# Kernel tuning notes

Hardware: AMD Instinct MI355X
Metric: run time of the kernel (lower is better)

The kernel has to match this reference:

```python
import jax, jax.numpy as jnp
import numpy as np

N = 50000   # number_of_nodes
E = 800000  # edges
K = 3       # Chebyshev order
C_IN = 64
C_OUT = 64


def _laplacian_weights(src, dst, w):
    # PyG ChebConv sym normalization with lambda_max=2: L_hat = -D^{-1/2} A D^{-1/2}
    deg = jax.ops.segment_sum(w, src, num_segments=N)
    dis = jnp.where(deg > 0, jax.lax.rsqrt(jnp.maximum(deg, 1e-12)), 0.0)
    return -dis[src] * w * dis[dst]


def _cheb(x, src, dst, lw, W, b):
    # x: [N, Cin], W: [K, Cin, Cout], b: [Cout]
    def prop(t):  # sparse L_hat @ t via gather + segment-sum scatter
        return jax.ops.segment_sum(lw[:, None] * t[src], dst, num_segments=N)
    Tx0 = x
    out = Tx0 @ W[0]
    Tx1 = prop(Tx0)
    out = out + Tx1 @ W[1]
    for k in range(2, W.shape[0]):  # Chebyshev recursion T_k = 2 L T_{k-1} - T_{k-2}
        Tx2 = 2.0 * prop(Tx1) - Tx0
        out = out + Tx2 @ W[k]
        Tx0, Tx1 = Tx1, Tx2
    return out + b


def setup_inputs() -> dict:
    key = jax.random.key(0)
    ks = jax.random.split(key, 20)
    inp = {
        "X": jax.random.normal(ks[0], (N, C_IN), jnp.float32),
        "edge_index": jax.random.randint(ks[1], (2, E), 0, N, jnp.int64),
        "edge_weight": jax.random.uniform(ks[2], (E,), jnp.float32),
        "H": jax.random.normal(ks[3], (N, C_OUT), jnp.float32),
    }
    names = ["xz", "hz", "xr", "hr", "xh", "hh"]
    for i, n in enumerate(names):
        cin = C_IN if n[0] == "x" else C_OUT
        inp[f"W_{n}"] = 0.1 * jax.random.normal(ks[4 + i], (K, cin, C_OUT), jnp.float32)
        inp[f"b_{n}"] = 0.1 * jax.random.normal(ks[10 + i], (C_OUT,), jnp.float32)
    return inp


def reference(X, edge_index, edge_weight, H,
              W_xz, W_hz, W_xr, W_hr, W_xh, W_hh,
              b_xz, b_hz, b_xr, b_hr, b_xh, b_hh):
    src, dst = edge_index[0], edge_index[1]
    lw = _laplacian_weights(src, dst, edge_weight)
    Z = jax.nn.sigmoid(_cheb(X, src, dst, lw, W_xz, b_xz) +
                       _cheb(H, src, dst, lw, W_hz, b_hz))
    R = jax.nn.sigmoid(_cheb(X, src, dst, lw, W_xr, b_xr) +
                       _cheb(H, src, dst, lw, W_hr, b_hr))
    H_tilde = jnp.tanh(_cheb(X, src, dst, lw, W_xh, b_xh) +
                       _cheb(H * R, src, dst, lw, W_hh, b_hh))
    H_new = Z * H + (1.0 - Z) * H_tilde
    return H_new
```

## Files before the change

kernel.cpp:

```cpp
#include <hip/hip_runtime.h>
#include <math.h>

#define CH 64

typedef __attribute__((ext_vector_type(8))) short bf16x8;
typedef __attribute__((ext_vector_type(4))) float f32x4;

static __device__ __forceinline__ float bf2f(ushort u) {
    union { unsigned int i; float f; } v; v.i = ((unsigned int)u) << 16; return v.f;
}
static __device__ __forceinline__ ushort f2bf(float f) {
    union { float f; unsigned int i; } v; v.f = f;
    unsigned int lsb = (v.i >> 16) & 1;
    v.i += 0x7fffu + lsb;
    return (ushort)(v.i >> 16);
}
static __device__ __forceinline__ unsigned int pack2(float a, float b) {
    return (unsigned int)f2bf(a) | ((unsigned int)f2bf(b) << 16);
}
static __device__ __forceinline__ float lo16(unsigned int u) { return bf2f((ushort)(u & 0xffffu)); }
static __device__ __forceinline__ float hi16(unsigned int u) { return bf2f((ushort)(u >> 16)); }


__global__ __launch_bounds__(256) void k_init(
    const int* __restrict__ src, const int* __restrict__ dst,
    const float* __restrict__ w,
    float* __restrict__ deg, int* __restrict__ cnt, int* __restrict__ erank, int E,
    const float4* __restrict__ X, const float4* __restrict__ H,
    ushort* __restrict__ XHb, int total4,
    const float* __restrict__ Wxz, const float* __restrict__ Whz,
    const float* __restrict__ Wxr, const float* __restrict__ Whr,
    const float* __restrict__ Wxh, const float* __restrict__ Whh,
    ushort* __restrict__ Bp, int bE, int bC)
{
    int b = blockIdx.x;
    int tid = threadIdx.x;
    if (b < bE) {
        int i = b * 256 + tid;
        if (i < E) {
            atomicAdd(&deg[src[i]], w[i]);
            erank[i] = atomicAdd(&cnt[dst[i]], 1);
        }
    } else if (b < bE + bC) {
        int i = (b - bE) * 256 + tid;
        if (i < total4) {
            float4 x = X[i], h = H[i];
            int node = i >> 4, c4 = i & 15;
            ushort4 xb, hb;
            xb.x = f2bf(x.x); xb.y = f2bf(x.y); xb.z = f2bf(x.z); xb.w = f2bf(x.w);
            hb.x = f2bf(h.x); hb.y = f2bf(h.y); hb.z = f2bf(h.z); hb.w = f2bf(h.w);
            *(ushort4*)(XHb + (size_t)node * 128 + c4 * 4)      = xb;
            *(ushort4*)(XHb + (size_t)node * 128 + 64 + c4 * 4) = hb;
        }
    } else {
        int mtg = b - bE - bC;
        int ct = tid >> 6;
        int lane = tid & 63;
        const float* W; int m, kt;
        if (mtg < 12)      { int l = mtg;      m = l >> 1; kt = l & 1; W = (m < 3) ? Wxz + m * 4096 : Whz + (m - 3) * 4096; }
        else if (mtg < 24) { int l = mtg - 12; m = l >> 1; kt = l & 1; W = (m < 3) ? Wxr + m * 4096 : Whr + (m - 3) * 4096; }
        else if (mtg < 30) { int l = mtg - 24; m = l >> 1; kt = l & 1; W = Wxh + m * 4096; }
        else               { int l = mtg - 30; m = l >> 1; kt = l & 1; W = Whh + m * 4096; }
        int cout = ct * 16 + (lane & 15);
        ushort* dstp = Bp + ((((mtg * 4) + ct) * 64 + lane) << 3);
        #pragma unroll
        for (int e = 0; e < 8; ++e) {
            int cin = kt * 32 + ((lane >> 4) << 3) + e;
            dstp[e] = f2bf(W[cin * 64 + cout]);
        }
    }
}


__global__ __launch_bounds__(256) void k_scanA(const int* __restrict__ cnt,
                                               int* __restrict__ rowptr,
                                               int* __restrict__ bsum, int N) {
    __shared__ int ts[256];
    int tid = threadIdx.x;
    int base = blockIdx.x * 2048 + tid * 8;
    int v[8]; int s = 0;
    #pragma unroll
    for (int k = 0; k < 8; ++k) { int i = base + k; v[k] = (i < N) ? cnt[i] : 0; s += v[k]; }
    ts[tid] = s;
    __syncthreads();
    for (int off = 1; off < 256; off <<= 1) {
        int t = (tid >= off) ? ts[tid - off] : 0;
        __syncthreads();
        ts[tid] += t;
        __syncthreads();
    }
    int run = ts[tid] - s;
    #pragma unroll
    for (int k = 0; k < 8; ++k) { int i = base + k; if (i < N) rowptr[i] = run; run += v[k]; }
    if (tid == 255) bsum[blockIdx.x] = ts[255];
}

__global__ void k_scanB(int* __restrict__ bsum, int B) {
    if (threadIdx.x == 0) {
        int acc = 0;
        for (int b = 0; b < B; ++b) { int t = bsum[b]; bsum[b] = acc; acc += t; }
        bsum[B] = acc;
    }
}

__global__ __launch_bounds__(256) void k_scanC(int* __restrict__ rowptr,
                                               const int* __restrict__ bsum,
                                               float* __restrict__ deg, int N, int B) {
    int base = blockIdx.x * 2048 + threadIdx.x * 8;
    int add = bsum[blockIdx.x];
    #pragma unroll
    for (int k = 0; k < 8; ++k) {
        int i = base + k;
        if (i < N) {
            rowptr[i] += add;
            float d = deg[i];
            deg[i] = (d > 0.f) ? rsqrtf(fmaxf(d, 1e-12f)) : 0.f;
        }
    }
    if (blockIdx.x == 0 && threadIdx.x == 0) rowptr[N] = bsum[B];
}


__global__ __launch_bounds__(256) void k_scatter(const int* __restrict__ src,
                                                 const int* __restrict__ dst,
                                                 const float* __restrict__ w,
                                                 const float* __restrict__ dis,
                                                 const int* __restrict__ rowptr,
                                                 const int* __restrict__ erank,
                                                 int2* __restrict__ emeta, int E) {
    int e = blockIdx.x * 256 + threadIdx.x;
    if (e < E) {
        int d = dst[e], s = src[e];
        int pos = rowptr[d] + erank[e];
        float lw = -dis[s] * w[e] * dis[d];
        emeta[pos] = make_int2(s, __float_as_int(lw));
    }
}


__global__ __launch_bounds__(256) void k_prop_dual(const int* __restrict__ rowptr,
                                                   const int2* __restrict__ emeta,
                                                   const unsigned int* __restrict__ t,
                                                   unsigned int* __restrict__ o, int N) {
    int wid = (blockIdx.x * 256 + threadIdx.x) >> 6;
    int lane = threadIdx.x & 63;
    if (wid >= N) return;
    int beg = rowptr[wid], end = rowptr[wid + 1];
    float ax = 0.f, ay = 0.f;
    int j = beg;
    for (; j + 3 < end; j += 4) {
        int2 m0 = emeta[j], m1 = emeta[j + 1], m2 = emeta[j + 2], m3 = emeta[j + 3];
        unsigned int p0 = t[(size_t)m0.x * 64 + lane];
        unsigned int p1 = t[(size_t)m1.x * 64 + lane];
        unsigned int p2 = t[(size_t)m2.x * 64 + lane];
        unsigned int p3 = t[(size_t)m3.x * 64 + lane];
        float l0 = __int_as_float(m0.y), l1 = __int_as_float(m1.y);
        float l2 = __int_as_float(m2.y), l3 = __int_as_float(m3.y);
        ax = fmaf(l0, lo16(p0), ax); ay = fmaf(l0, hi16(p0), ay);
        ax = fmaf(l1, lo16(p1), ax); ay = fmaf(l1, hi16(p1), ay);
        ax = fmaf(l2, lo16(p2), ax); ay = fmaf(l2, hi16(p2), ay);
        ax = fmaf(l3, lo16(p3), ax); ay = fmaf(l3, hi16(p3), ay);
    }
    for (; j < end; ++j) {
        int2 m = emeta[j];
        unsigned int p = t[(size_t)m.x * 64 + lane];
        float l = __int_as_float(m.y);
        ax = fmaf(l, lo16(p), ax); ay = fmaf(l, hi16(p), ay);
    }
    o[(size_t)wid * 64 + lane] = pack2(ax, ay);
}

__global__ __launch_bounds__(256) void k_prop_dual2(const int* __restrict__ rowptr,
                                                    const int2* __restrict__ emeta,
                                                    const unsigned int* __restrict__ t,
                                                    const unsigned int* __restrict__ t0,
                                                    unsigned int* __restrict__ o, int N) {
    int wid = (blockIdx.x * 256 + threadIdx.x) >> 6;
    int lane = threadIdx.x & 63;
    if (wid >= N) return;
    int beg = rowptr[wid], end = rowptr[wid + 1];
    float ax = 0.f, ay = 0.f;
    int j = beg;
    for (; j + 3 < end; j += 4) {
        int2 m0 = emeta[j], m1 = emeta[j + 1], m2 = emeta[j + 2], m3 = emeta[j + 3];
        unsigned int p0 = t[(size_t)m0.x * 64 + lane];
        unsigned int p1 = t[(size_t)m1.x * 64 + lane];
        unsigned int p2 = t[(size_t)m2.x * 64 + lane];
        unsigned int p3 = t[(size_t)m3.x * 64 + lane];
        float l0 = __int_as_float(m0.y), l1 = __int_as_float(m1.y);
        float l2 = __int_as_float(m2.y), l3 = __int_as_float(m3.y);
        ax = fmaf(l0, lo16(p0), ax); ay = fmaf(l0, hi16(p0), ay);
        ax = fmaf(l1, lo16(p1), ax); ay = fmaf(l1, hi16(p1), ay);
        ax = fmaf(l2, lo16(p2), ax); ay = fmaf(l2, hi16(p2), ay);
        ax = fmaf(l3, lo16(p3), ax); ay = fmaf(l3, hi16(p3), ay);
    }
    for (; j < end; ++j) {
        int2 m = emeta[j];
        unsigned int p = t[(size_t)m.x * 64 + lane];
        float l = __int_as_float(m.y);
        ax = fmaf(l, lo16(p), ax); ay = fmaf(l, hi16(p), ay);
    }
    size_t oi = (size_t)wid * 64 + lane;
    unsigned int z = t0[oi];
    o[oi] = pack2(2.f * ax - lo16(z), 2.f * ay - hi16(z));
}


__global__ __launch_bounds__(256) void k_prop1(const int* __restrict__ rowptr,
                                               const int2* __restrict__ emeta,
                                               const unsigned int* __restrict__ t,
                                               unsigned int* __restrict__ out, int N) {
    int wv = (blockIdx.x * 256 + threadIdx.x) >> 6;
    int lane = threadIdx.x & 63;
    int node = wv * 2 + (lane >> 5);
    int sl = lane & 31;
    if (node >= N) return;
    int beg = rowptr[node], end = rowptr[node + 1];
    float ax = 0.f, ay = 0.f;
    int j = beg;
    for (; j + 3 < end; j += 4) {
        int2 m0 = emeta[j], m1 = emeta[j + 1], m2 = emeta[j + 2], m3 = emeta[j + 3];
        unsigned int p0 = t[(size_t)m0.x * 32 + sl];
        unsigned int p1 = t[(size_t)m1.x * 32 + sl];
        unsigned int p2 = t[(size_t)m2.x * 32 + sl];
        unsigned int p3 = t[(size_t)m3.x * 32 + sl];
        float l0 = __int_as_float(m0.y), l1 = __int_as_float(m1.y);
        float l2 = __int_as_float(m2.y), l3 = __int_as_float(m3.y);
        ax = fmaf(l0, lo16(p0), ax); ay = fmaf(l0, hi16(p0), ay);
        ax = fmaf(l1, lo16(p1), ax); ay = fmaf(l1, hi16(p1), ay);
        ax = fmaf(l2, lo16(p2), ax); ay = fmaf(l2, hi16(p2), ay);
        ax = fmaf(l3, lo16(p3), ax); ay = fmaf(l3, hi16(p3), ay);
    }
    for (; j < end; ++j) {
        int2 m = emeta[j];
        unsigned int p = t[(size_t)m.x * 32 + sl];
        float l = __int_as_float(m.y);
        ax = fmaf(l, lo16(p), ax); ay = fmaf(l, hi16(p), ay);
    }
    out[(size_t)node * 32 + sl] = pack2(ax, ay);
}

__global__ __launch_bounds__(256) void k_prop2(const int* __restrict__ rowptr,
                                               const int2* __restrict__ emeta,
                                               const unsigned int* __restrict__ t,
                                               const unsigned int* __restrict__ t0,
                                               unsigned int* __restrict__ out, int N) {
    int wv = (blockIdx.x * 256 + threadIdx.x) >> 6;
    int lane = threadIdx.x & 63;
    int node = wv * 2 + (lane >> 5);
    int sl = lane & 31;
    if (node >= N) return;
    int beg = rowptr[node], end = rowptr[node + 1];
    float ax = 0.f, ay = 0.f;
    int j = beg;
    for (; j + 3 < end; j += 4) {
        int2 m0 = emeta[j], m1 = emeta[j + 1], m2 = emeta[j + 2], m3 = emeta[j + 3];
        unsigned int p0 = t[(size_t)m0.x * 32 + sl];
        unsigned int p1 = t[(size_t)m1.x * 32 + sl];
        unsigned int p2 = t[(size_t)m2.x * 32 + sl];
        unsigned int p3 = t[(size_t)m3.x * 32 + sl];
        float l0 = __int_as_float(m0.y), l1 = __int_as_float(m1.y);
        float l2 = __int_as_float(m2.y), l3 = __int_as_float(m3.y);
        ax = fmaf(l0, lo16(p0), ax); ay = fmaf(l0, hi16(p0), ay);
        ax = fmaf(l1, lo16(p1), ax); ay = fmaf(l1, hi16(p1), ay);
        ax = fmaf(l2, lo16(p2), ax); ay = fmaf(l2, hi16(p2), ay);
        ax = fmaf(l3, lo16(p3), ax); ay = fmaf(l3, hi16(p3), ay);
    }
    for (; j < end; ++j) {
        int2 m = emeta[j];
        unsigned int p = t[(size_t)m.x * 32 + sl];
        float l = __int_as_float(m.y);
        ax = fmaf(l, lo16(p), ax); ay = fmaf(l, hi16(p), ay);
    }
    size_t oi = (size_t)node * 32 + sl;
    unsigned int z = t0[oi];
    out[oi] = pack2(2.f * ax - lo16(z), 2.f * ay - hi16(z));
}


static __device__ __forceinline__ bf16x8 ldA(const ushort* __restrict__ t, int stride,
                                             int row0, int lane, int kt, int N) {
    int row = row0 + (lane & 15);
    bf16x8 v = {};
    if (row < N) v = *(const bf16x8*)(t + (size_t)row * stride + kt * 32 + ((lane >> 4) << 3));
    return v;
}
static __device__ __forceinline__ bf16x8 ldB(const ushort* __restrict__ bp,
                                             int mt, int ct, int lane) {
    return *(const bf16x8*)(bp + ((((mt * 4) + ct) * 64 + lane) << 3));
}

#define MFMA(a, b, c) __builtin_amdgcn_mfma_f32_16x16x32_bf16(a, b, c, 0, 0, 0)


__global__ __launch_bounds__(256) void k_gA(
    const ushort* __restrict__ XHb, const ushort* __restrict__ T1xh, const ushort* __restrict__ T2xh,
    const ushort* __restrict__ Bp,
    const float* __restrict__ bxz, const float* __restrict__ bhz,
    const float* __restrict__ bxr, const float* __restrict__ bhr,
    const float* __restrict__ bxh,
    const float* __restrict__ H,
    ushort* __restrict__ Zb, ushort* __restrict__ HRb, float* __restrict__ preH, int N)
{
    int wid = blockIdx.x * 4 + (threadIdx.x >> 6);
    int lane = threadIdx.x & 63;
    int row0 = wid * 32;
    if (row0 >= N) return;

    f32x4 accZ[2][4], accR[2][4], accH[2][4];
    #pragma unroll
    for (int ct = 0; ct < 4; ++ct) {
        int col = ct * 16 + (lane & 15);
        float bz = bxz[col] + bhz[col];
        float br = bxr[col] + bhr[col];
        float bh = bxh[col];
        #pragma unroll
        for (int rt = 0; rt < 2; ++rt) {
            accZ[rt][ct] = (f32x4){bz, bz, bz, bz};
            accR[rt][ct] = (f32x4){br, br, br, br};
            accH[rt][ct] = (f32x4){bh, bh, bh, bh};
        }
    }

    const ushort* ins[6] = { XHb, T1xh, T2xh, XHb + 64, T1xh + 64, T2xh + 64 };

    #pragma unroll
    for (int m = 0; m < 6; ++m) {
        #pragma unroll
        for (int kt = 0; kt < 2; ++kt) {
            bf16x8 a0 = ldA(ins[m], 128, row0,      lane, kt, N);
            bf16x8 a1 = ldA(ins[m], 128, row0 + 16, lane, kt, N);
            int mt = m * 2 + kt;
            #pragma unroll
            for (int ct = 0; ct < 4; ++ct) {
                bf16x8 bz8 = ldB(Bp, mt, ct, lane);
                accZ[0][ct] = MFMA(a0, bz8, accZ[0][ct]);
                accZ[1][ct] = MFMA(a1, bz8, accZ[1][ct]);
                bf16x8 br8 = ldB(Bp, 12 + mt, ct, lane);
                accR[0][ct] = MFMA(a0, br8, accR[0][ct]);
                accR[1][ct] = MFMA(a1, br8, accR[1][ct]);
                if (m < 3) {
                    bf16x8 bh8 = ldB(Bp, 24 + mt, ct, lane);
                    accH[0][ct] = MFMA(a0, bh8, accH[0][ct]);
                    accH[1][ct] = MFMA(a1, bh8, accH[1][ct]);
                }
            }
        }
    }

    #pragma unroll
    for (int rt = 0; rt < 2; ++rt) {
        #pragma unroll
        for (int ct = 0; ct < 4; ++ct) {
            int col = ct * 16 + (lane & 15);
            #pragma unroll
            for (int r = 0; r < 4; ++r) {
                int row = row0 + rt * 16 + ((lane >> 4) << 2) + r;
                if (row < N) {
                    int o = row * CH + col;
                    float z = 1.f / (1.f + expf(-accZ[rt][ct][r]));
                    float rr = 1.f / (1.f + expf(-accR[rt][ct][r]));
                    float h = H[o];
                    Zb[o] = f2bf(z);
                    HRb[o] = f2bf(h * rr);
                    preH[o] = accH[rt][ct][r];
                }
            }
        }
    }
}


__global__ __launch_bounds__(256) void k_gB(
    const ushort* __restrict__ HRb, const ushort* __restrict__ T1, const ushort* __restrict__ T2,
    const ushort* __restrict__ Bp, const float* __restrict__ bhh,
    const ushort* __restrict__ Zb, const float* __restrict__ H,
    float* __restrict__ out , int N)
{
    int wid = blockIdx.x * 4 + (threadIdx.x >> 6);
    int lane = threadIdx.x & 63;
    int row0 = wid * 32;
    if (row0 >= N) return;

    f32x4 acc[2][4];
    #pragma unroll
    for (int ct = 0; ct < 4; ++ct) {
        int col = ct * 16 + (lane & 15);
        float bh = bhh[col];
        #pragma unroll
        for (int rt = 0; rt < 2; ++rt) acc[rt][ct] = (f32x4){bh, bh, bh, bh};
    }

    const ushort* ins[3] = { HRb, T1, T2 };

    #pragma unroll
    for (int m = 0; m < 3; ++m) {
        #pragma unroll
        for (int kt = 0; kt < 2; ++kt) {
            bf16x8 a0 = ldA(ins[m], 64, row0,      lane, kt, N);
            bf16x8 a1 = ldA(ins[m], 64, row0 + 16, lane, kt, N);
            int mt = 30 + m * 2 + kt;
            #pragma unroll
            for (int ct = 0; ct < 4; ++ct) {
                bf16x8 b8 = ldB(Bp, mt, ct, lane);
                acc[0][ct] = MFMA(a0, b8, acc[0][ct]);
                acc[1][ct] = MFMA(a1, b8, acc[1][ct]);
            }
        }
    }

    #pragma unroll
    for (int rt = 0; rt < 2; ++rt) {
        #pragma unroll
        for (int ct = 0; ct < 4; ++ct) {
            int col = ct * 16 + (lane & 15);
            #pragma unroll
            for (int r = 0; r < 4; ++r) {
                int row = row0 + rt * 16 + ((lane >> 4) << 2) + r;
                if (row < N) {
                    int o = row * CH + col;
                    float pre = acc[rt][ct][r] + out[o];
                    float z = bf2f(Zb[o]);
                    float h = H[o];
                    out[o] = z * h + (1.f - z) * tanhf(pre);
                }
            }
        }
    }
}


extern "C" void kernel_launch(void* const* d_in, const int* in_sizes, int n_in,
                              void* d_out, int out_size, void* d_ws, size_t ws_size,
                              hipStream_t stream) {
    const float* X   = (const float*)d_in[0];
    const int*   ei  = (const int*)d_in[1];
    const float* ew  = (const float*)d_in[2];
    const float* H   = (const float*)d_in[3];
    const float* Wxz = (const float*)d_in[4];
    const float* bxz = (const float*)d_in[5];
    const float* Whz = (const float*)d_in[6];
    const float* bhz = (const float*)d_in[7];
    const float* Wxr = (const float*)d_in[8];
    const float* bxr = (const float*)d_in[9];
    const float* Whr = (const float*)d_in[10];
    const float* bhr = (const float*)d_in[11];
    const float* Wxh = (const float*)d_in[12];
    const float* bxh = (const float*)d_in[13];
    const float* Whh = (const float*)d_in[14];
    const float* bhh = (const float*)d_in[15];

    const int N = in_sizes[0] / CH;
    const int E = in_sizes[2];
    const long long NC = (long long)N * CH;

    const int* srcI = ei;
    const int* dstI = ei + E;

    char* p = (char*)d_ws;
    auto alloc = [&](size_t bytes) { char* r = p; p += (bytes + 255) & ~(size_t)255; return r; };
    int*    rowptr = (int*)alloc((size_t)(N + 1) * 4);
    int2*   emeta  = (int2*)alloc((size_t)E * 8);
    int*    erank  = (int*)alloc((size_t)E * 4);
    float*  deg    = (float*)alloc((size_t)N * 8);
    int*    cnt    = (int*)(deg + N);
    int*    bsum   = (int*)alloc(256 * 4);
    ushort* Bp     = (ushort*)alloc((size_t)36 * 4 * 64 * 8 * 2);
    ushort* XHb    = (ushort*)alloc((size_t)NC * 2 * 2);
    ushort* T1xh   = (ushort*)alloc((size_t)NC * 2 * 2);
    ushort* T2xh   = (ushort*)alloc((size_t)NC * 2 * 2);
    ushort* HRb    = (ushort*)alloc((size_t)NC * 2);
    ushort* T1r    = (ushort*)alloc((size_t)NC * 2);
    ushort* T2r    = (ushort*)alloc((size_t)NC * 2);
    ushort* Zb     = (ushort*)alloc((size_t)NC * 2);
    float*  preH   = (float*)d_out;

    const int total4 = (int)(NC / 4);
    const int bE = (E + 255) / 256;
    const int bC = (total4 + 255) / 256;
    const int B  = (N + 2047) / 2048;
    const int bW = (int)((N * 64 + 255) / 256);
    const int bW2 = (int)((((N + 1) / 2) * 64 + 255) / 256);
    const int nW = (N + 31) / 32;
    const int bG = (nW + 3) / 4;

    hipMemsetAsync(deg, 0, (size_t)N * 8, stream);
    k_init<<<bE + bC + 36, 256, 0, stream>>>(srcI, dstI, ew, deg, cnt, erank, E,
                                             (const float4*)X, (const float4*)H, XHb, total4,
                                             Wxz, Whz, Wxr, Whr, Wxh, Whh, Bp, bE, bC);

    k_scanA<<<B, 256, 0, stream>>>(cnt, rowptr, bsum, N);
    k_scanB<<<1, 64, 0, stream>>>(bsum, B);
    k_scanC<<<B, 256, 0, stream>>>(rowptr, bsum, deg, N, B);

    k_scatter<<<bE, 256, 0, stream>>>(srcI, dstI, ew, deg, rowptr, erank, emeta, E);

    k_prop_dual <<<bW, 256, 0, stream>>>(rowptr, emeta, (const unsigned int*)XHb,
                                         (unsigned int*)T1xh, N);
    k_prop_dual2<<<bW, 256, 0, stream>>>(rowptr, emeta, (const unsigned int*)T1xh,
                                         (const unsigned int*)XHb, (unsigned int*)T2xh, N);

    k_gA<<<bG, 256, 0, stream>>>(XHb, T1xh, T2xh, Bp,
                                 bxz, bhz, bxr, bhr, bxh,
                                 H, Zb, HRb, preH, N);

    k_prop1<<<bW2, 256, 0, stream>>>(rowptr, emeta, (const unsigned int*)HRb,
                                     (unsigned int*)T1r, N);
    k_prop2<<<bW2, 256, 0, stream>>>(rowptr, emeta, (const unsigned int*)T1r,
                                     (const unsigned int*)HRb, (unsigned int*)T2r, N);

    k_gB<<<bG, 256, 0, stream>>>(HRb, T1r, T2r, Bp, bhh, Zb, H, (float*)d_out, N);
}
```

Baseline: 297.3 us.

## Unroll SpMM edge loops by 8 with nontemporal metadata loads, bf16 preH, shuffle scan

The four CSR propagation kernels now unroll the edge loop by 8 instead of 4 and fetch the edge metadata with nontemporal loads, aiming for more gathers in flight and less cache pollution. The intermediate pre-activation for the candidate state moves from fp32 in the output buffer to a separate bf16 workspace array, halving that traffic at some precision cost. The single-thread block-sum scan becomes a 64-lane wavefront shuffle scan. That scan only covers up to 64 block sums, which is enough for N=50000 (25 blocks).

```diff
diff --git a/kernel.cpp b/kernel.cpp
--- a/kernel.cpp
+++ b/kernel.cpp
@@ -5,6 +5,7 @@
 
 typedef __attribute__((ext_vector_type(8))) short bf16x8;
 typedef __attribute__((ext_vector_type(4))) float f32x4;
+typedef __attribute__((ext_vector_type(2))) int int2v;
 
 static __device__ __forceinline__ float bf2f(ushort u) {
     union { unsigned int i; float f; } v; v.i = ((unsigned int)u) << 16; return v.f;
@@ -96,11 +97,16 @@
 }
 
 __global__ void k_scanB(int* __restrict__ bsum, int B) {
-    if (threadIdx.x == 0) {
-        int acc = 0;
-        for (int b = 0; b < B; ++b) { int t = bsum[b]; bsum[b] = acc; acc += t; }
-        bsum[B] = acc;
-    }
+    int lane = threadIdx.x;
+    int v = (lane < B) ? bsum[lane] : 0;
+    int incl = v;
+    #pragma unroll
+    for (int off = 1; off < 64; off <<= 1) {
+        int t = __shfl_up(incl, off, 64);
+        if (lane >= off) incl += t;
+    }
+    if (lane < B) bsum[lane] = incl - v;
+    if (lane == B - 1) bsum[B] = incl;
 }
 
 __global__ __launch_bounds__(256) void k_scanC(int* __restrict__ rowptr,
@@ -138,8 +144,13 @@
 }
 
 
+#define DUAL_STEP(mm) { \
+    unsigned int p = t[(size_t)(mm).x * 64 + lane]; \
+    float l = __int_as_float((mm).y); \
+    ax = fmaf(l, lo16(p), ax); ay = fmaf(l, hi16(p), ay); }
+
 __global__ __launch_bounds__(256) void k_prop_dual(const int* __restrict__ rowptr,
-                                                   const int2* __restrict__ emeta,
+                                                   const int2v* __restrict__ emeta,
                                                    const unsigned int* __restrict__ t,
                                                    unsigned int* __restrict__ o, int N) {
     int wid = (blockIdx.x * 256 + threadIdx.x) >> 6;
@@ -148,30 +159,27 @@
     int beg = rowptr[wid], end = rowptr[wid + 1];
     float ax = 0.f, ay = 0.f;
     int j = beg;
-    for (; j + 3 < end; j += 4) {
-        int2 m0 = emeta[j], m1 = emeta[j + 1], m2 = emeta[j + 2], m3 = emeta[j + 3];
-        unsigned int p0 = t[(size_t)m0.x * 64 + lane];
-        unsigned int p1 = t[(size_t)m1.x * 64 + lane];
-        unsigned int p2 = t[(size_t)m2.x * 64 + lane];
-        unsigned int p3 = t[(size_t)m3.x * 64 + lane];
-        float l0 = __int_as_float(m0.y), l1 = __int_as_float(m1.y);
-        float l2 = __int_as_float(m2.y), l3 = __int_as_float(m3.y);
-        ax = fmaf(l0, lo16(p0), ax); ay = fmaf(l0, hi16(p0), ay);
-        ax = fmaf(l1, lo16(p1), ax); ay = fmaf(l1, hi16(p1), ay);
-        ax = fmaf(l2, lo16(p2), ax); ay = fmaf(l2, hi16(p2), ay);
-        ax = fmaf(l3, lo16(p3), ax); ay = fmaf(l3, hi16(p3), ay);
+    for (; j + 7 < end; j += 8) {
+        int2v m0 = __builtin_nontemporal_load(&emeta[j]);
+        int2v m1 = __builtin_nontemporal_load(&emeta[j + 1]);
+        int2v m2 = __builtin_nontemporal_load(&emeta[j + 2]);
+        int2v m3 = __builtin_nontemporal_load(&emeta[j + 3]);
+        int2v m4 = __builtin_nontemporal_load(&emeta[j + 4]);
+        int2v m5 = __builtin_nontemporal_load(&emeta[j + 5]);
+        int2v m6 = __builtin_nontemporal_load(&emeta[j + 6]);
+        int2v m7 = __builtin_nontemporal_load(&emeta[j + 7]);
+        DUAL_STEP(m0) DUAL_STEP(m1) DUAL_STEP(m2) DUAL_STEP(m3)
+        DUAL_STEP(m4) DUAL_STEP(m5) DUAL_STEP(m6) DUAL_STEP(m7)
     }
     for (; j < end; ++j) {
-        int2 m = emeta[j];
-        unsigned int p = t[(size_t)m.x * 64 + lane];
-        float l = __int_as_float(m.y);
-        ax = fmaf(l, lo16(p), ax); ay = fmaf(l, hi16(p), ay);
+        int2v m = __builtin_nontemporal_load(&emeta[j]);
+        DUAL_STEP(m)
     }
     o[(size_t)wid * 64 + lane] = pack2(ax, ay);
 }
 
 __global__ __launch_bounds__(256) void k_prop_dual2(const int* __restrict__ rowptr,
-                                                    const int2* __restrict__ emeta,
+                                                    const int2v* __restrict__ emeta,
                                                     const unsigned int* __restrict__ t,
                                                     const unsigned int* __restrict__ t0,
                                                     unsigned int* __restrict__ o, int N) {
@@ -181,24 +189,21 @@
     int beg = rowptr[wid], end = rowptr[wid + 1];
     float ax = 0.f, ay = 0.f;
     int j = beg;
-    for (; j + 3 < end; j += 4) {
-        int2 m0 = emeta[j], m1 = emeta[j + 1], m2 = emeta[j + 2], m3 = emeta[j + 3];
-        unsigned int p0 = t[(size_t)m0.x * 64 + lane];
-        unsigned int p1 = t[(size_t)m1.x * 64 + lane];
-        unsigned int p2 = t[(size_t)m2.x * 64 + lane];
-        unsigned int p3 = t[(size_t)m3.x * 64 + lane];
-        float l0 = __int_as_float(m0.y), l1 = __int_as_float(m1.y);
-        float l2 = __int_as_float(m2.y), l3 = __int_as_float(m3.y);
-        ax = fmaf(l0, lo16(p0), ax); ay = fmaf(l0, hi16(p0), ay);
-        ax = fmaf(l1, lo16(p1), ax); ay = fmaf(l1, hi16(p1), ay);
-        ax = fmaf(l2, lo16(p2), ax); ay = fmaf(l2, hi16(p2), ay);
-        ax = fmaf(l3, lo16(p3), ax); ay = fmaf(l3, hi16(p3), ay);
+    for (; j + 7 < end; j += 8) {
+        int2v m0 = __builtin_nontemporal_load(&emeta[j]);
+        int2v m1 = __builtin_nontemporal_load(&emeta[j + 1]);
+        int2v m2 = __builtin_nontemporal_load(&emeta[j + 2]);
+        int2v m3 = __builtin_nontemporal_load(&emeta[j + 3]);
+        int2v m4 = __builtin_nontemporal_load(&emeta[j + 4]);
+        int2v m5 = __builtin_nontemporal_load(&emeta[j + 5]);
+        int2v m6 = __builtin_nontemporal_load(&emeta[j + 6]);
+        int2v m7 = __builtin_nontemporal_load(&emeta[j + 7]);
+        DUAL_STEP(m0) DUAL_STEP(m1) DUAL_STEP(m2) DUAL_STEP(m3)
+        DUAL_STEP(m4) DUAL_STEP(m5) DUAL_STEP(m6) DUAL_STEP(m7)
     }
     for (; j < end; ++j) {
-        int2 m = emeta[j];
-        unsigned int p = t[(size_t)m.x * 64 + lane];
-        float l = __int_as_float(m.y);
-        ax = fmaf(l, lo16(p), ax); ay = fmaf(l, hi16(p), ay);
+        int2v m = __builtin_nontemporal_load(&emeta[j]);
+        DUAL_STEP(m)
     }
     size_t oi = (size_t)wid * 64 + lane;
     unsigned int z = t0[oi];
@@ -206,8 +211,13 @@
 }
 
 
+#define HR_STEP(mm) { \
+    unsigned int p = t[(size_t)(mm).x * 32 + sl]; \
+    float l = __int_as_float((mm).y); \
+    ax = fmaf(l, lo16(p), ax); ay = fmaf(l, hi16(p), ay); }
+
 __global__ __launch_bounds__(256) void k_prop1(const int* __restrict__ rowptr,
-                                               const int2* __restrict__ emeta,
+                                               const int2v* __restrict__ emeta,
                                                const unsigned int* __restrict__ t,
                                                unsigned int* __restrict__ out, int N) {
     int wv = (blockIdx.x * 256 + threadIdx.x) >> 6;
@@ -218,30 +228,27 @@
     int beg = rowptr[node], end = rowptr[node + 1];
     float ax = 0.f, ay = 0.f;
     int j = beg;
-    for (; j + 3 < end; j += 4) {
-        int2 m0 = emeta[j], m1 = emeta[j + 1], m2 = emeta[j + 2], m3 = emeta[j + 3];
-        unsigned int p0 = t[(size_t)m0.x * 32 + sl];
-        unsigned int p1 = t[(size_t)m1.x * 32 + sl];
-        unsigned int p2 = t[(size_t)m2.x * 32 + sl];
-        unsigned int p3 = t[(size_t)m3.x * 32 + sl];
-        float l0 = __int_as_float(m0.y), l1 = __int_as_float(m1.y);
-        float l2 = __int_as_float(m2.y), l3 = __int_as_float(m3.y);
-        ax = fmaf(l0, lo16(p0), ax); ay = fmaf(l0, hi16(p0), ay);
-        ax = fmaf(l1, lo16(p1), ax); ay = fmaf(l1, hi16(p1), ay);
-        ax = fmaf(l2, lo16(p2), ax); ay = fmaf(l2, hi16(p2), ay);
-        ax = fmaf(l3, lo16(p3), ax); ay = fmaf(l3, hi16(p3), ay);
+    for (; j + 7 < end; j += 8) {
+        int2v m0 = __builtin_nontemporal_load(&emeta[j]);
+        int2v m1 = __builtin_nontemporal_load(&emeta[j + 1]);
+        int2v m2 = __builtin_nontemporal_load(&emeta[j + 2]);
+        int2v m3 = __builtin_nontemporal_load(&emeta[j + 3]);
+        int2v m4 = __builtin_nontemporal_load(&emeta[j + 4]);
+        int2v m5 = __builtin_nontemporal_load(&emeta[j + 5]);
+        int2v m6 = __builtin_nontemporal_load(&emeta[j + 6]);
+        int2v m7 = __builtin_nontemporal_load(&emeta[j + 7]);
+        HR_STEP(m0) HR_STEP(m1) HR_STEP(m2) HR_STEP(m3)
+        HR_STEP(m4) HR_STEP(m5) HR_STEP(m6) HR_STEP(m7)
     }
     for (; j < end; ++j) {
-        int2 m = emeta[j];
-        unsigned int p = t[(size_t)m.x * 32 + sl];
-        float l = __int_as_float(m.y);
-        ax = fmaf(l, lo16(p), ax); ay = fmaf(l, hi16(p), ay);
+        int2v m = __builtin_nontemporal_load(&emeta[j]);
+        HR_STEP(m)
     }
     out[(size_t)node * 32 + sl] = pack2(ax, ay);
 }
 
 __global__ __launch_bounds__(256) void k_prop2(const int* __restrict__ rowptr,
-                                               const int2* __restrict__ emeta,
+                                               const int2v* __restrict__ emeta,
                                                const unsigned int* __restrict__ t,
                                                const unsigned int* __restrict__ t0,
                                                unsigned int* __restrict__ out, int N) {
@@ -253,24 +260,21 @@
     int beg = rowptr[node], end = rowptr[node + 1];
     float ax = 0.f, ay = 0.f;
     int j = beg;
-    for (; j + 3 < end; j += 4) {
-        int2 m0 = emeta[j], m1 = emeta[j + 1], m2 = emeta[j + 2], m3 = emeta[j + 3];
-        unsigned int p0 = t[(size_t)m0.x * 32 + sl];
-        unsigned int p1 = t[(size_t)m1.x * 32 + sl];
-        unsigned int p2 = t[(size_t)m2.x * 32 + sl];
-        unsigned int p3 = t[(size_t)m3.x * 32 + sl];
-        float l0 = __int_as_float(m0.y), l1 = __int_as_float(m1.y);
-        float l2 = __int_as_float(m2.y), l3 = __int_as_float(m3.y);
-        ax = fmaf(l0, lo16(p0), ax); ay = fmaf(l0, hi16(p0), ay);
-        ax = fmaf(l1, lo16(p1), ax); ay = fmaf(l1, hi16(p1), ay);
-        ax = fmaf(l2, lo16(p2), ax); ay = fmaf(l2, hi16(p2), ay);
-        ax = fmaf(l3, lo16(p3), ax); ay = fmaf(l3, hi16(p3), ay);
+    for (; j + 7 < end; j += 8) {
+        int2v m0 = __builtin_nontemporal_load(&emeta[j]);
+        int2v m1 = __builtin_nontemporal_load(&emeta[j + 1]);
+        int2v m2 = __builtin_nontemporal_load(&emeta[j + 2]);
+        int2v m3 = __builtin_nontemporal_load(&emeta[j + 3]);
+        int2v m4 = __builtin_nontemporal_load(&emeta[j + 4]);
+        int2v m5 = __builtin_nontemporal_load(&emeta[j + 5]);
+        int2v m6 = __builtin_nontemporal_load(&emeta[j + 6]);
+        int2v m7 = __builtin_nontemporal_load(&emeta[j + 7]);
+        HR_STEP(m0) HR_STEP(m1) HR_STEP(m2) HR_STEP(m3)
+        HR_STEP(m4) HR_STEP(m5) HR_STEP(m6) HR_STEP(m7)
     }
     for (; j < end; ++j) {
-        int2 m = emeta[j];
-        unsigned int p = t[(size_t)m.x * 32 + sl];
-        float l = __int_as_float(m.y);
-        ax = fmaf(l, lo16(p), ax); ay = fmaf(l, hi16(p), ay);
+        int2v m = __builtin_nontemporal_load(&emeta[j]);
+        HR_STEP(m)
     }
     size_t oi = (size_t)node * 32 + sl;
     unsigned int z = t0[oi];
@@ -300,7 +304,7 @@
     const float* __restrict__ bxr, const float* __restrict__ bhr,
     const float* __restrict__ bxh,
     const float* __restrict__ H,
-    ushort* __restrict__ Zb, ushort* __restrict__ HRb, float* __restrict__ preH, int N)
+    ushort* __restrict__ Zb, ushort* __restrict__ HRb, ushort* __restrict__ preHb, int N)
 {
     int wid = blockIdx.x * 4 + (threadIdx.x >> 6);
     int lane = threadIdx.x & 63;
@@ -363,7 +367,7 @@
                     float h = H[o];
                     Zb[o] = f2bf(z);
                     HRb[o] = f2bf(h * rr);
-                    preH[o] = accH[rt][ct][r];
+                    preHb[o] = f2bf(accH[rt][ct][r]);
                 }
             }
         }
@@ -375,7 +379,7 @@
     const ushort* __restrict__ HRb, const ushort* __restrict__ T1, const ushort* __restrict__ T2,
     const ushort* __restrict__ Bp, const float* __restrict__ bhh,
     const ushort* __restrict__ Zb, const float* __restrict__ H,
-    float* __restrict__ out , int N)
+    const ushort* __restrict__ preHb, float* __restrict__ out, int N)
 {
     int wid = blockIdx.x * 4 + (threadIdx.x >> 6);
     int lane = threadIdx.x & 63;
@@ -419,7 +423,7 @@
                 int row = row0 + rt * 16 + ((lane >> 4) << 2) + r;
                 if (row < N) {
                     int o = row * CH + col;
-                    float pre = acc[rt][ct][r] + out[o];
+                    float pre = acc[rt][ct][r] + bf2f(preHb[o]);
                     float z = bf2f(Zb[o]);
                     float h = H[o];
                     out[o] = z * h + (1.f - z) * tanhf(pre);
@@ -473,7 +477,7 @@
     ushort* T1r    = (ushort*)alloc((size_t)NC * 2);
     ushort* T2r    = (ushort*)alloc((size_t)NC * 2);
     ushort* Zb     = (ushort*)alloc((size_t)NC * 2);
-    float*  preH   = (float*)d_out;
+    ushort* preHb  = (ushort*)alloc((size_t)NC * 2);
 
     const int total4 = (int)(NC / 4);
     const int bE = (E + 255) / 256;
@@ -495,19 +499,19 @@
 
     k_scatter<<<bE, 256, 0, stream>>>(srcI, dstI, ew, deg, rowptr, erank, emeta, E);
 
-    k_prop_dual <<<bW, 256, 0, stream>>>(rowptr, emeta, (const unsigned int*)XHb,
+    k_prop_dual <<<bW, 256, 0, stream>>>(rowptr, (const int2v*)emeta, (const unsigned int*)XHb,
                                          (unsigned int*)T1xh, N);
-    k_prop_dual2<<<bW, 256, 0, stream>>>(rowptr, emeta, (const unsigned int*)T1xh,
+    k_prop_dual2<<<bW, 256, 0, stream>>>(rowptr, (const int2v*)emeta, (const unsigned int*)T1xh,
                                          (const unsigned int*)XHb, (unsigned int*)T2xh, N);
 
     k_gA<<<bG, 256, 0, stream>>>(XHb, T1xh, T2xh, Bp,
                                  bxz, bhz, bxr, bhr, bxh,
-                                 H, Zb, HRb, preH, N);
-
-    k_prop1<<<bW2, 256, 0, stream>>>(rowptr, emeta, (const unsigned int*)HRb,
+                                 H, Zb, HRb, preHb, N);
+
+    k_prop1<<<bW2, 256, 0, stream>>>(rowptr, (const int2v*)emeta, (const unsigned int*)HRb,
                                      (unsigned int*)T1r, N);
-    k_prop2<<<bW2, 256, 0, stream>>>(rowptr, emeta, (const unsigned int*)T1r,
+    k_prop2<<<bW2, 256, 0, stream>>>(rowptr, (const int2v*)emeta, (const unsigned int*)T1r,
                                      (const unsigned int*)HRb, (unsigned int*)T2r, N);
 
-    k_gB<<<bG, 256, 0, stream>>>(HRb, T1r, T2r, Bp, bhh, Zb, H, (float*)d_out, N);
-}
+    k_gB<<<bG, 256, 0, stream>>>(HRb, T1r, T2r, Bp, bhh, Zb, H, preHb, (float*)d_out, N);
+}
```

New measurement: 331.7 us. 1.12x slower.
